# Kernel optimization log

Measured on AMD Instinct MI355X. Metric: run time of the kernel, lower is better.

The kernel has to match this reference:

```python
import jax, jax.numpy as jnp
import numpy as np

N = 8192
F_IN = 256
F_OUT = 128
NEG_BIG = -9.0e15


def setup_inputs() -> dict:
    key = jax.random.key(0)
    k1, k2, k3, k4 = jax.random.split(key, 4)
    x = jax.random.normal(k1, (N, F_IN), dtype=jnp.float32)
    W = jax.random.normal(k2, (F_IN, F_OUT), dtype=jnp.float32) * 0.05
    a = jax.random.normal(k3, (2 * F_OUT, 1), dtype=jnp.float32) * 0.05
    adj = jax.random.randint(k4, (N, N), 0, 2, dtype=jnp.int32)
    return {"x": x, "W": W, "a": a, "adj": adj}


def reference(x, W, a, adj):
    # h = x @ W : [N, F_OUT]
    h = x @ W
    # Original builds [N, N, 2F] concat then matmuls with a. Since
    # a_input[i,j] = concat(h_i, h_j), the score is separable:
    # (a_input @ a)[i,j] = h_i . a[:F] + h_j . a[F:]
    a1 = a[:F_OUT, 0]   # [F_OUT]
    a2 = a[F_OUT:, 0]   # [F_OUT]
    s1 = h @ a1         # [N]
    s2 = h @ a2         # [N]
    e = jax.nn.leaky_relu(s1[:, None] + s2[None, :], negative_slope=0.2)
    e = jnp.where(adj > 0, e, jnp.float32(NEG_BIG))
    attention = jax.nn.softmax(e, axis=1)   # [N, N]
    h_prime = attention @ h                 # [N, F_OUT]
    return jax.nn.elu(h_prime)
```

## Files before the change

### kernel.cpp

```cpp
#include <hip/hip_runtime.h>
#include <math.h>

#define NN 8192

typedef __attribute__((ext_vector_type(8))) short short8;
typedef __attribute__((ext_vector_type(4))) short short4v;
typedef __attribute__((ext_vector_type(4))) float f32x4;
typedef __attribute__((ext_vector_type(4))) int int4v;

#define L2E 1.4426950408889634f

typedef __attribute__((address_space(3))) unsigned lds_u32;
typedef __attribute__((address_space(1))) unsigned g_u32;

__device__ __forceinline__ void gll16(const void* g, void* l) {
    __builtin_amdgcn_global_load_lds((const g_u32*)g, (lds_u32*)l, 16, 0, 0);
}

__device__ __forceinline__ short f2bf(float f) {
    union { float f; unsigned u; } v; v.f = f;
    unsigned r = v.u + 0x7fffu + ((v.u >> 16) & 1u);
    return (short)(r >> 16);
}

__device__ __forceinline__ f32x4 zero4() {
    f32x4 v; v[0] = 0.f; v[1] = 0.f; v[2] = 0.f; v[3] = 0.f; return v;
}

__global__ void k0_wt(const float* __restrict__ W, short* __restrict__ WT) {
    int idx = blockIdx.x * 256 + threadIdx.x;
    if (idx < 256 * 128) {
        int k = idx & 255;
        int f = idx >> 8;
        WT[f * 256 + k] = f2bf(W[k * 128 + f]);
    }
}

__global__ __launch_bounds__(128) void k1_h(
        const float* __restrict__ x, const short* __restrict__ WT,
        const float* __restrict__ a, short* __restrict__ hT,
        float* __restrict__ E1p, float* __restrict__ E1n,
        float* __restrict__ E2p, float* __restrict__ E2n) {
    const int w = threadIdx.x >> 6;
    const int l = threadIdx.x & 63;
    const int quad = l >> 4;
    const int fr = l & 15;
    const int i0 = blockIdx.x * 32 + w * 16;

    f32x4 acc[8];
#pragma unroll
    for (int t = 0; t < 8; ++t) acc[t] = zero4();

    const float* xrow = x + (size_t)(i0 + fr) * 256;
#pragma unroll
    for (int kk = 0; kk < 8; ++kk) {
        const int k0 = kk * 32 + quad * 8;
        f32x4 xa = *(const f32x4*)(xrow + k0);
        f32x4 xb = *(const f32x4*)(xrow + k0 + 4);
        short8 av;
#pragma unroll
        for (int e = 0; e < 4; ++e) { av[e] = f2bf(xa[e]); av[4 + e] = f2bf(xb[e]); }
#pragma unroll
        for (int t = 0; t < 8; ++t) {
            short8 bv = *(const short8*)(WT + (t * 16 + fr) * 256 + k0);
            acc[t] = __builtin_amdgcn_mfma_f32_16x16x32_bf16(av, bv, acc[t], 0, 0, 0);
        }
    }

    float s1p[4] = {0.f, 0.f, 0.f, 0.f};
    float s2p[4] = {0.f, 0.f, 0.f, 0.f};
#pragma unroll
    for (int t = 0; t < 8; ++t) {
        float a1v = a[t * 16 + fr];
        float a2v = a[128 + t * 16 + fr];
#pragma unroll
        for (int r = 0; r < 4; ++r) {
            s1p[r] += acc[t][r] * a1v;
            s2p[r] += acc[t][r] * a2v;
        }
    }
#pragma unroll
    for (int r = 0; r < 4; ++r) {
#pragma unroll
        for (int m = 1; m < 16; m <<= 1) {
            s1p[r] += __shfl_xor(s1p[r], m, 64);
            s2p[r] += __shfl_xor(s2p[r], m, 64);
        }
    }
    if (fr == 0) {
#pragma unroll
        for (int r = 0; r < 4; ++r) {
            const int i = i0 + quad * 4 + r;
            const float v1 = s1p[r];
            const float v2 = s2p[r];
            E1p[i] = exp2f(v1 * L2E);
            E1n[i] = exp2f(v1 * (0.2f * L2E));
            E2p[i] = exp2f(v2 * L2E);
            E2n[i] = exp2f(v2 * (0.2f * L2E));
        }
    }

#pragma unroll
    for (int t = 0; t < 8; ++t) {
        short4v hv;
#pragma unroll
        for (int r = 0; r < 4; ++r) hv[r] = f2bf(acc[t][r]);
        *(short4v*)(hT + (size_t)(t * 16 + fr) * NN + i0 + quad * 4) = hv;
    }
}

template<int JSPLIT, bool PARTIAL>
__global__ __launch_bounds__(256, 2) void k2_attn(
        const int* __restrict__ adj, const short* __restrict__ hT,
        const float* __restrict__ E1p, const float* __restrict__ E1n,
        const float* __restrict__ E2p, const float* __restrict__ E2n,
        float* __restrict__ pvp, float* __restrict__ zp,
        float* __restrict__ out) {
    constexpr int JW = NN / JSPLIT;
    constexpr int NSTEP = JW / 64;
    __shared__ __align__(16) char lds_c[49408];

    const int tid = threadIdx.x;
    const int w = tid >> 6;
    const int l = tid & 63;
    const int quad = l >> 4;
    const int fr = l & 15;
    const int rh = w >> 1;
    const int wj = w & 1;
    const int rb = blockIdx.x / JSPLIT;
    const int jb = blockIdx.x % JSPLIT;
    const int r32 = rb * 32;
    const int jbb = jb * JW;

    const int myrow = r32 + rh * 16 + fr;
    const float Rp = E1p[myrow];
    const float Rn = E1n[myrow];
    const float thr = 1.0f / Rp;

    const char* hsrc[4];
    {
        const char* hbase = (const char*)hT;
#pragma unroll
        for (int p = 0; p < 4; ++p) {
            const int o = p * 4096 + tid * 16;
            const int row = o >> 7;
            const int colb = o & 127;
            hsrc[p] = hbase + (size_t)row * (NN * 2) + (size_t)jbb * 2
                    + (colb ^ ((row & 7) << 4));
        }
    }
    const char* asrc[2];
    {
        const char* abase = (const char*)adj;
#pragma unroll
        for (int p = 0; p < 2; ++p) {
            const int o = p * 4096 + tid * 16;
            const int row = o >> 8;
            const int colb = o & 255;
            asrc[p] = abase + (size_t)(r32 + row) * (NN * 4) + (size_t)jbb * 4
                    + (colb ^ ((row & 7) << 4));
        }
    }

    auto STAGE = [&](int jt, int buf) {
        char* hd = lds_c + buf * 16384 + w * 1024;
        char* ad = lds_c + 32768 + buf * 8192 + w * 1024;
        const size_t hof = (size_t)jt * 128;
        const size_t aof = (size_t)jt * 256;
#pragma unroll
        for (int p = 0; p < 4; ++p) gll16(hsrc[p] + hof, hd + p * 4096);
#pragma unroll
        for (int p = 0; p < 2; ++p) gll16(asrc[p] + aof, ad + p * 4096);
    };

    f32x4 cE[4], nE[4];
    auto loadE2 = [&](int jt, f32x4* E) {
        const int j = jbb + jt * 64 + wj * 32 + quad * 8;
        E[0] = *(const f32x4*)(E2p + j);
        E[1] = *(const f32x4*)(E2p + j + 4);
        E[2] = *(const f32x4*)(E2n + j);
        E[3] = *(const f32x4*)(E2n + j + 4);
    };

    f32x4 acc[8];
#pragma unroll
    for (int t = 0; t < 8; ++t) acc[t] = zero4();
    float zacc = 0.f;

    STAGE(0, 0);
    loadE2(0, cE);
    __syncthreads();

    int cur = 0;
    for (int jt = 0; jt < NSTEP; ++jt) {
        if (jt + 1 < NSTEP) {
            STAGE(jt + 1, cur ^ 1);
            loadE2(jt + 1, nE);
        }
        __builtin_amdgcn_sched_barrier(0);

        const char* hb = lds_c + cur * 16384;
        const char* ab = lds_c + 32768 + cur * 8192;

        const int arow = rh * 16 + fr;
        const unsigned aswz = (unsigned)((arow & 7) << 4);
        const unsigned al = (unsigned)(arow * 256 + wj * 128 + quad * 32);
        int4v g0 = *(const int4v*)(ab + (al ^ aswz));
        int4v g1 = *(const int4v*)(ab + ((al + 16) ^ aswz));

        short8 pa;
        {
            float zs = 0.f;
#pragma unroll
            for (int e = 0; e < 8; ++e) {
                const float cp = (e < 4) ? cE[0][e & 3] : cE[1][e & 3];
                const float cn = (e < 4) ? cE[2][e & 3] : cE[3][e & 3];
                const int gv = (e < 4) ? g0[e & 3] : g1[e & 3];
                const bool hi = cp >= thr;
                const float fc = hi ? cp : cn;
                const float rf = hi ? Rp : Rn;
                float p = fc * rf;
                p = (gv > 0) ? p : 0.f;
                zs += p;
                pa[e] = f2bf(p);
            }
            zacc += zs;
        }

#pragma unroll
        for (int t = 0; t < 8; ++t) {
            const int hrow = t * 16 + fr;
            const short8 bv = *(const short8*)(
                hb + ((unsigned)(hrow * 128 + wj * 64 + quad * 16) ^ ((hrow & 7) << 4)));
            acc[t] = __builtin_amdgcn_mfma_f32_16x16x32_bf16(pa, bv, acc[t], 0, 0, 0);
        }

        __syncthreads();
        cur ^= 1;
        cE[0] = nE[0]; cE[1] = nE[1]; cE[2] = nE[2]; cE[3] = nE[3];
    }

    zacc += __shfl_xor(zacc, 16, 64);
    zacc += __shfl_xor(zacc, 32, 64);
    float* zb = (float*)(lds_c + 49152);
    if (l < 16) zb[w * 16 + l] = zacc;

    float* red = (float*)lds_c;
    if (wj == 1) {
#pragma unroll
        for (int t = 0; t < 8; ++t)
            *(f32x4*)(red + rh * 2048 + t * 256 + l * 4) = acc[t];
    }
    __syncthreads();

    if (wj == 0) {
#pragma unroll
        for (int t = 0; t < 8; ++t)
            acc[t] += *(const f32x4*)(red + rh * 2048 + t * 256 + l * 4);
#pragma unroll
        for (int r = 0; r < 4; ++r) {
            const int irow = quad * 4 + r;
            const float z = zb[rh * 32 + irow] + zb[rh * 32 + 16 + irow];
            const int grow = r32 + rh * 16 + irow;
            if (PARTIAL) {
                if (fr == 0) zp[(size_t)jb * NN + grow] = z;
                float* orow = pvp + ((size_t)jb * NN + grow) * 128;
#pragma unroll
                for (int t = 0; t < 8; ++t) orow[t * 16 + fr] = acc[t][r];
            } else {
                const float inv = 1.0f / z;
                float* orow = out + (size_t)grow * 128;
#pragma unroll
                for (int t = 0; t < 8; ++t) {
                    float v = acc[t][r] * inv;
                    orow[t * 16 + fr] = (v > 0.f) ? v : expm1f(v);
                }
            }
        }
    }
}

__global__ __launch_bounds__(256) void k3_fin(
        const float* __restrict__ pvp, const float* __restrict__ zp,
        float* __restrict__ out, int jsplit) {
    const int idx = blockIdx.x * 256 + threadIdx.x;
    const int row = idx >> 5;
    const int c = (idx & 31) << 2;
    f32x4 s = zero4();
    float z = 0.f;
    for (int p = 0; p < jsplit; ++p) {
        s += *(const f32x4*)(pvp + ((size_t)p * NN + row) * 128 + c);
        z += zp[(size_t)p * NN + row];
    }
    const float inv = 1.0f / z;
    f32x4 o;
#pragma unroll
    for (int e = 0; e < 4; ++e) {
        float v = s[e] * inv;
        o[e] = (v > 0.f) ? v : expm1f(v);
    }
    *(f32x4*)(out + (size_t)row * 128 + c) = o;
}

extern "C" void kernel_launch(void* const* d_in, const int* in_sizes, int n_in,
                              void* d_out, int out_size, void* d_ws, size_t ws_size,
                              hipStream_t stream) {
    const float* x   = (const float*)d_in[0];
    const float* W   = (const float*)d_in[1];
    const float* a   = (const float*)d_in[2];
    const int*   adj = (const int*)d_in[3];
    float* out = (float*)d_out;

    char* ws = (char*)d_ws;
    const size_t MB = 1024 * 1024;
    short* hT  = (short*)ws;
    float* E1p = (float*)(ws + 2 * MB);
    float* E1n = (float*)(ws + 2 * MB + 32768);
    float* E2p = (float*)(ws + 2 * MB + 65536);
    float* E2n = (float*)(ws + 2 * MB + 98304);
    short* WT  = (short*)(ws + 2 * MB + 131072);
    const size_t base = 2 * MB + 196608;

    const size_t need2 = base + 2 * ((size_t)NN * 128 * 4) + 2 * ((size_t)NN * 4);
    const bool js2 = (ws_size >= need2);

    float* pvp = (float*)(ws + base);
    float* zp  = (float*)(ws + base + (size_t)2 * NN * 128 * 4);

    k0_wt<<<128, 256, 0, stream>>>(W, WT);
    k1_h<<<256, 128, 0, stream>>>(x, WT, a, hT, E1p, E1n, E2p, E2n);

    if (js2) {
        k2_attn<2, true><<<512, 256, 0, stream>>>(adj, hT, E1p, E1n, E2p, E2n, pvp, zp, nullptr);
        k3_fin<<<1024, 256, 0, stream>>>(pvp, zp, out, 2);
    } else {
        k2_attn<1, false><<<256, 256, 0, stream>>>(adj, hT, E1p, E1n, E2p, E2n, nullptr, nullptr, out);
    }
}
```

Baseline: 97.00 us.

## Triple-buffer attention tiles via LDS and compute exp2 in-loop instead of precomputed factors

Moves the attention kernel from a double buffer to a three-stage LDS ring, using manual vmcnt waits and raw barriers so global-to-LDS loads run further ahead of the MFMA work. The per-column score vector is now staged into LDS with the other tiles, replacing per-thread global register loads. Precomputed exp factors (four arrays) become two scaled score arrays, and leaky-relu plus exp2 are computed per element in the loop. This trades fewer memory streams and better latency hiding for more transcendental work per element, more LDS per block (which may affect occupancy), and a hand-tuned vmcnt count that must match the number of issued loads.

```diff
diff --git a/kernel.cpp b/kernel.cpp
--- a/kernel.cpp
+++ b/kernel.cpp
@@ -39,8 +39,7 @@
 __global__ __launch_bounds__(128) void k1_h(
         const float* __restrict__ x, const short* __restrict__ WT,
         const float* __restrict__ a, short* __restrict__ hT,
-        float* __restrict__ E1p, float* __restrict__ E1n,
-        float* __restrict__ E2p, float* __restrict__ E2n) {
+        float* __restrict__ s1L2E, float* __restrict__ s2L2E) {
     const int w = threadIdx.x >> 6;
     const int l = threadIdx.x & 63;
     const int quad = l >> 4;
@@ -91,12 +90,8 @@
 #pragma unroll
         for (int r = 0; r < 4; ++r) {
             const int i = i0 + quad * 4 + r;
-            const float v1 = s1p[r];
-            const float v2 = s2p[r];
-            E1p[i] = exp2f(v1 * L2E);
-            E1n[i] = exp2f(v1 * (0.2f * L2E));
-            E2p[i] = exp2f(v2 * L2E);
-            E2n[i] = exp2f(v2 * (0.2f * L2E));
+            s1L2E[i] = s1p[r] * L2E;
+            s2L2E[i] = s2p[r] * L2E;
         }
     }
 
@@ -112,13 +107,13 @@
 template<int JSPLIT, bool PARTIAL>
 __global__ __launch_bounds__(256, 2) void k2_attn(
         const int* __restrict__ adj, const short* __restrict__ hT,
-        const float* __restrict__ E1p, const float* __restrict__ E1n,
-        const float* __restrict__ E2p, const float* __restrict__ E2n,
+        const float* __restrict__ s1g, const float* __restrict__ s2g,
         float* __restrict__ pvp, float* __restrict__ zp,
         float* __restrict__ out) {
     constexpr int JW = NN / JSPLIT;
     constexpr int NSTEP = JW / 64;
-    __shared__ __align__(16) char lds_c[49408];
+    constexpr int BUFB = 25600;
+    __shared__ __align__(16) char lds_c[3 * BUFB + 256];
 
     const int tid = threadIdx.x;
     const int w = tid >> 6;
@@ -132,10 +127,7 @@
     const int r32 = rb * 32;
     const int jbb = jb * JW;
 
-    const int myrow = r32 + rh * 16 + fr;
-    const float Rp = E1p[myrow];
-    const float Rn = E1n[myrow];
-    const float thr = 1.0f / Rp;
+    const float S = s1g[r32 + rh * 16 + fr];
 
     const char* hsrc[4];
     {
@@ -161,25 +153,20 @@
                     + (colb ^ ((row & 7) << 4));
         }
     }
+    const char* csrc = (const char*)s2g + (size_t)jbb * 4 + (l < 16 ? l * 16 : 240);
 
     auto STAGE = [&](int jt, int buf) {
-        char* hd = lds_c + buf * 16384 + w * 1024;
-        char* ad = lds_c + 32768 + buf * 8192 + w * 1024;
+        jt = (jt < NSTEP) ? jt : NSTEP - 1;
+        char* hd = lds_c + buf * BUFB + w * 1024;
+        char* ad = lds_c + buf * BUFB + 16384 + w * 1024;
+        char* cd = lds_c + buf * BUFB + 24576;
         const size_t hof = (size_t)jt * 128;
         const size_t aof = (size_t)jt * 256;
 #pragma unroll
         for (int p = 0; p < 4; ++p) gll16(hsrc[p] + hof, hd + p * 4096);
 #pragma unroll
         for (int p = 0; p < 2; ++p) gll16(asrc[p] + aof, ad + p * 4096);
-    };
-
-    f32x4 cE[4], nE[4];
-    auto loadE2 = [&](int jt, f32x4* E) {
-        const int j = jbb + jt * 64 + wj * 32 + quad * 8;
-        E[0] = *(const f32x4*)(E2p + j);
-        E[1] = *(const f32x4*)(E2p + j + 4);
-        E[2] = *(const f32x4*)(E2n + j);
-        E[3] = *(const f32x4*)(E2n + j + 4);
+        gll16(csrc + aof, cd);
     };
 
     f32x4 acc[8];
@@ -187,40 +174,36 @@
     for (int t = 0; t < 8; ++t) acc[t] = zero4();
     float zacc = 0.f;
 
-    STAGE(0, 0);
-    loadE2(0, cE);
-    __syncthreads();
+    STAGE(0, 0); STAGE(1, 1); STAGE(2, 2);
 
     int cur = 0;
-    for (int jt = 0; jt < NSTEP; ++jt) {
-        if (jt + 1 < NSTEP) {
-            STAGE(jt + 1, cur ^ 1);
-            loadE2(jt + 1, nE);
-        }
+    for (int t = 0; t < NSTEP; ++t) {
+        asm volatile("s_waitcnt vmcnt(14)" ::: "memory");
+        __builtin_amdgcn_s_barrier();
         __builtin_amdgcn_sched_barrier(0);
 
-        const char* hb = lds_c + cur * 16384;
-        const char* ab = lds_c + 32768 + cur * 8192;
+        const char* hb = lds_c + cur * BUFB;
+        const char* ab = lds_c + cur * BUFB + 16384;
+        const float* cb = (const float*)(lds_c + cur * BUFB + 24576);
 
         const int arow = rh * 16 + fr;
         const unsigned aswz = (unsigned)((arow & 7) << 4);
         const unsigned al = (unsigned)(arow * 256 + wj * 128 + quad * 32);
-        int4v g0 = *(const int4v*)(ab + (al ^ aswz));
-        int4v g1 = *(const int4v*)(ab + ((al + 16) ^ aswz));
+        const int4v g0 = *(const int4v*)(ab + (al ^ aswz));
+        const int4v g1 = *(const int4v*)(ab + ((al + 16) ^ aswz));
+        const f32x4 c0 = *(const f32x4*)(cb + wj * 32 + quad * 8);
+        const f32x4 c1 = *(const f32x4*)(cb + wj * 32 + quad * 8 + 4);
 
         short8 pa;
         {
             float zs = 0.f;
 #pragma unroll
             for (int e = 0; e < 8; ++e) {
-                const float cp = (e < 4) ? cE[0][e & 3] : cE[1][e & 3];
-                const float cn = (e < 4) ? cE[2][e & 3] : cE[3][e & 3];
+                const float cv = (e < 4) ? c0[e & 3] : c1[e & 3];
                 const int gv = (e < 4) ? g0[e & 3] : g1[e & 3];
-                const bool hi = cp >= thr;
-                const float fc = hi ? cp : cn;
-                const float rf = hi ? Rp : Rn;
-                float p = fc * rf;
-                p = (gv > 0) ? p : 0.f;
+                const float u = S + cv;
+                const float tt = fmaxf(u, 0.2f * u);
+                const float p = (gv > 0) ? exp2f(tt) : 0.f;
                 zs += p;
                 pa[e] = f2bf(p);
             }
@@ -228,21 +211,27 @@
         }
 
 #pragma unroll
-        for (int t = 0; t < 8; ++t) {
-            const int hrow = t * 16 + fr;
+        for (int t8 = 0; t8 < 8; ++t8) {
+            const int hrow = t8 * 16 + fr;
             const short8 bv = *(const short8*)(
                 hb + ((unsigned)(hrow * 128 + wj * 64 + quad * 16) ^ ((hrow & 7) << 4)));
-            acc[t] = __builtin_amdgcn_mfma_f32_16x16x32_bf16(pa, bv, acc[t], 0, 0, 0);
-        }
-
-        __syncthreads();
-        cur ^= 1;
-        cE[0] = nE[0]; cE[1] = nE[1]; cE[2] = nE[2]; cE[3] = nE[3];
-    }
+            acc[t8] = __builtin_amdgcn_mfma_f32_16x16x32_bf16(pa, bv, acc[t8], 0, 0, 0);
+        }
+
+        __builtin_amdgcn_sched_barrier(0);
+        asm volatile("" ::: "memory");
+        __builtin_amdgcn_s_barrier();
+
+        STAGE(t + 3, cur);
+        cur = (cur == 2) ? 0 : cur + 1;
+    }
+
+    asm volatile("s_waitcnt vmcnt(0)" ::: "memory");
+    __syncthreads();
 
     zacc += __shfl_xor(zacc, 16, 64);
     zacc += __shfl_xor(zacc, 32, 64);
-    float* zb = (float*)(lds_c + 49152);
+    float* zb = (float*)(lds_c + 3 * BUFB);
     if (l < 16) zb[w * 16 + l] = zacc;
 
     float* red = (float*)lds_c;
@@ -313,13 +302,11 @@
 
     char* ws = (char*)d_ws;
     const size_t MB = 1024 * 1024;
-    short* hT  = (short*)ws;
-    float* E1p = (float*)(ws + 2 * MB);
-    float* E1n = (float*)(ws + 2 * MB + 32768);
-    float* E2p = (float*)(ws + 2 * MB + 65536);
-    float* E2n = (float*)(ws + 2 * MB + 98304);
-    short* WT  = (short*)(ws + 2 * MB + 131072);
-    const size_t base = 2 * MB + 196608;
+    short* hT    = (short*)ws;
+    float* s1L2E = (float*)(ws + 2 * MB);
+    float* s2L2E = (float*)(ws + 2 * MB + 32768);
+    short* WT    = (short*)(ws + 2 * MB + 65536);
+    const size_t base = 2 * MB + 131072;
 
     const size_t need2 = base + 2 * ((size_t)NN * 128 * 4) + 2 * ((size_t)NN * 4);
     const bool js2 = (ws_size >= need2);
@@ -328,12 +315,12 @@
     float* zp  = (float*)(ws + base + (size_t)2 * NN * 128 * 4);
 
     k0_wt<<<128, 256, 0, stream>>>(W, WT);
-    k1_h<<<256, 128, 0, stream>>>(x, WT, a, hT, E1p, E1n, E2p, E2n);
+    k1_h<<<256, 128, 0, stream>>>(x, WT, a, hT, s1L2E, s2L2E);
 
     if (js2) {
-        k2_attn<2, true><<<512, 256, 0, stream>>>(adj, hT, E1p, E1n, E2p, E2n, pvp, zp, nullptr);
+        k2_attn<2, true><<<512, 256, 0, stream>>>(adj, hT, s1L2E, s2L2E, pvp, zp, nullptr);
         k3_fin<<<1024, 256, 0, stream>>>(pvp, zp, out, 2);
     } else {
-        k2_attn<1, false><<<256, 256, 0, stream>>>(adj, hT, E1p, E1n, E2p, E2n, nullptr, nullptr, out);
-    }
-}
+        k2_attn<1, false><<<256, 256, 0, stream>>>(adj, hT, s1L2E, s2L2E, nullptr, nullptr, out);
+    }
+}
```

Measured after the change: 94.73 us. -2.3%, faster.
